# Performance work log

Hardware: AMD Instinct MI355X
Metric: run time of the kernel (lower is better)

The kernel has to match this reference:

```python
import jax, jax.numpy as jnp
import numpy as np

SCALE = 0.1
NUM_AA = 21  # num_aa + 1
NUM_RBF = 64
D_MIN, D_MAX = 0.0, 20.0
EPS = 1e-8


def _rbf(d):
    # d: [E] -> [E, NUM_RBF]
    mu = jnp.linspace(D_MIN, D_MAX, NUM_RBF, dtype=d.dtype)
    sigma = (D_MAX - D_MIN) / NUM_RBF
    return jnp.exp(-(((d[:, None] - mu) / sigma) ** 2))


def setup_inputs() -> dict:
    key = jax.random.key(0)
    k1, k2, k3, k4, k5 = jax.random.split(key, 5)
    N, E = 10000, 320000
    return {
        "decoded_atom14": jax.random.normal(k1, (N, 14, 3), dtype=jnp.float32),
        "rot": jax.random.normal(k2, (N, 3, 3), dtype=jnp.float32),
        "trans": jax.random.normal(k3, (N, 3), dtype=jnp.float32),
        "decoded_seq_logits": jax.random.normal(k4, (N, NUM_AA), dtype=jnp.float32),
        "edge_index": jax.random.randint(k5, (2, E), 0, N, dtype=jnp.int64)
        if jax.config.jax_enable_x64 else jax.random.randint(k5, (2, E), 0, N, dtype=jnp.int32),
    }


def reference(decoded_atom14, rot, trans, decoded_seq_logits, edge_index):
    E = edge_index.shape[1]
    dst = edge_index[0]
    src = edge_index[1]

    atom14 = decoded_atom14 * SCALE          # [N,14,3]
    t = trans * SCALE                        # [N,3] (scale_translation)

    seq = jnp.argmax(decoded_seq_logits, axis=-1)          # [N]
    src_seq = jax.nn.one_hot(seq[src], NUM_AA, dtype=jnp.float32)  # [E,21]
    dst_seq = jax.nn.one_hot(seq[dst], NUM_AA, dtype=jnp.float32)  # [E,21]

    X_ca = atom14[:, 1, :]                                  # [N,3]
    edge_dists = jnp.linalg.norm(X_ca[dst] - X_ca[src], axis=-1)   # [E]
    edge_rbf = _rbf(edge_dists)                             # [E,64]

    # invert_apply: R^T (x - t), per node, broadcast over 14 atoms
    local = jnp.einsum("nji,naj->nai", rot, atom14 - t[:, None, :])  # [N,14,3]
    src_atom14_local = local[src]                           # [E,14,3]
    dst_atom14_in_src_local = jnp.einsum(
        "eji,eaj->eai", rot[src], atom14[dst] - t[src][:, None, :]
    )                                                       # [E,14,3]

    # 14x14 pairwise distances (eps added to diff coords, as in original)
    diff = src_atom14_local[:, :, None, :] - dst_atom14_in_src_local[:, None, :, :] + EPS
    pair_dist = jnp.linalg.norm(diff, axis=-1)              # [E,14,14]

    return jnp.concatenate(
        [
            jnp.ones((E, 1), dtype=jnp.float32),
            src_seq,
            dst_seq,
            edge_rbf,
            src_atom14_local.reshape(E, -1),
            dst_atom14_in_src_local.reshape(E, -1),
            pair_dist.reshape(E, -1),
        ],
        axis=-1,
    ).astype(jnp.float32)
```

## Files before the change

### kernel.cpp

```cpp
#include <hip/hip_runtime.h>
#include <math.h>

#define NUM_AA   21
#define OUT_DIM  387
#define SCALE    0.1f
#define EPS_C    1e-8f
#define EPB      32
#define TPB      1024

typedef float v4f __attribute__((ext_vector_type(4)));

__global__ __launch_bounds__(256) void node_pre_kernel(
    const float* __restrict__ A, const float* __restrict__ R,
    const float* __restrict__ T, const float* __restrict__ LG,
    float* __restrict__ WS, int N)
{
    const int n = blockIdx.x * 256 + threadIdx.x;
    if (n >= N) return;

    float a14[42];
    #pragma unroll
    for (int k = 0; k < 42; ++k) a14[k] = A[(size_t)n * 42 + k] * SCALE;
    float rot[9];
    #pragma unroll
    for (int k = 0; k < 9; ++k) rot[k] = R[(size_t)n * 9 + k];
    const float t0 = T[(size_t)n * 3 + 0] * SCALE;
    const float t1 = T[(size_t)n * 3 + 1] * SCALE;
    const float t2 = T[(size_t)n * 3 + 2] * SCALE;

    const float* lg = LG + (size_t)n * NUM_AA;
    float best = lg[0]; int bi = 0;
    #pragma unroll
    for (int j = 1; j < NUM_AA; ++j) {
        float v = lg[j];
        if (v > best) { best = v; bi = j; }
    }

    float* S = WS + (size_t)n * 64;
    float* D = WS + (size_t)N * 64 + (size_t)n * 48;

    #pragma unroll
    for (int a = 0; a < 14; ++a) {
        const float x0 = a14[a * 3 + 0] - t0;
        const float x1 = a14[a * 3 + 1] - t1;
        const float x2 = a14[a * 3 + 2] - t2;
        #pragma unroll
        for (int i = 0; i < 3; ++i)
            S[a * 3 + i] = rot[i] * x0 + rot[3 + i] * x1 + rot[6 + i] * x2;
    }
    #pragma unroll
    for (int k = 0; k < 9; ++k) S[42 + k] = rot[k];
    S[51] = t0; S[52] = t1; S[53] = t2;
    S[54] = a14[3]; S[55] = a14[4]; S[56] = a14[5];
    S[57] = (float)bi;
    #pragma unroll
    for (int k = 58; k < 64; ++k) S[k] = 0.f;

    #pragma unroll
    for (int k = 0; k < 42; ++k) D[k] = a14[k];
    D[42] = a14[3]; D[43] = a14[4]; D[44] = a14[5];
    D[45] = (float)bi;
    D[46] = 0.f; D[47] = 0.f;
}

__device__ __forceinline__ void edge_phase1(const float* __restrict__ gs,
                                            float* __restrict__ row, int lane)
{
    {
        const float dx = gs[106] - gs[54];
        const float dy = gs[107] - gs[55];
        const float dz = gs[108] - gs[56];
        const float dca = __builtin_amdgcn_sqrtf(dx * dx + dy * dy + dz * dz);
        const float mu  = (float)lane * (20.0f / 63.0f);
        const float z   = (dca - mu) * 3.2f;
        row[43 + lane] = __expf(-z * z);
    }
    const int seqS = (int)gs[57];
    const int seqD = (int)gs[109];
    if (lane == 21) row[0] = 1.0f;
    if (lane < 21) {
        row[1  + lane] = (lane == seqS) ? 1.0f : 0.0f;
        row[22 + lane] = (lane == seqD) ? 1.0f : 0.0f;
    }
    if (lane < 42) {
        const int a = lane / 3;
        const int i = lane - a * 3;
        const float r0 = gs[42 + i], r1 = gs[45 + i], r2 = gs[48 + i];
        const float locD = r0 * (gs[64 + a * 3 + 0] - gs[51])
                         + r1 * (gs[64 + a * 3 + 1] - gs[52])
                         + r2 * (gs[64 + a * 3 + 2] - gs[53]);
        row[107 + lane] = gs[lane];
        row[149 + lane] = locD;
    }
}

__device__ __forceinline__ void edge_phase2(float* __restrict__ row, int lane)
{
    #pragma unroll
    for (int k = 0; k < 4; ++k) {
        const int p = lane + k * 64;
        if (p < 196) {
            const unsigned a = (unsigned)p / 14u;
            const unsigned b = (unsigned)p - a * 14u;
            const float ddx = row[107 + a * 3 + 0] - row[149 + b * 3 + 0] + EPS_C;
            const float ddy = row[107 + a * 3 + 1] - row[149 + b * 3 + 1] + EPS_C;
            const float ddz = row[107 + a * 3 + 2] - row[149 + b * 3 + 2] + EPS_C;
            row[191 + p] = __builtin_amdgcn_sqrtf(ddx * ddx + ddy * ddy + ddz * ddz);
        }
    }
}

__global__ __launch_bounds__(1024, 2) void edge_feat_kernel(
    const int*   __restrict__ EI,
    const float* __restrict__ WS,
    float* __restrict__ out,
    int E, int N)
{
    __shared__ __align__(16) float rowsh[EPB * OUT_DIM];
    __shared__ __align__(16) float gsh[16][224];

    const int wv   = threadIdx.x >> 6;
    const int lane = threadIdx.x & 63;
    const int eb   = blockIdx.x * EPB + wv * 2;

    int dst0, src0, dst1, src1;
    if (eb + 1 < E) {
        const int2 d = *reinterpret_cast<const int2*>(EI + eb);
        const int2 s = *reinterpret_cast<const int2*>(EI + E + eb);
        dst0 = d.x; dst1 = d.y; src0 = s.x; src1 = s.y;
    } else {
        const int e0c = (eb < E) ? eb : E - 1;
        dst0 = EI[e0c]; src0 = EI[E + e0c];
        dst1 = dst0; src1 = src0;
    }

    float* row0 = rowsh + (size_t)(wv * 2) * OUT_DIM;
    float* row1 = row0 + OUT_DIM;
    float* gs   = gsh[wv];

    {
        const int k   = (lane >= 28) ? 1 : 0;
        const int lr  = lane - k * 28;
        const bool isD = lr >= 16;
        const int sub = isD ? lr - 16 : lr;
        const int node = isD ? (k ? dst1 : dst0) : (k ? src1 : src0);
        const float* p = isD
            ? WS + (size_t)N * 64 + (size_t)node * 48 + sub * 4
            : WS + (size_t)node * 64 + sub * 4;
        if (lane < 56) {
            const v4f v = *reinterpret_cast<const v4f*>(p);
            *reinterpret_cast<v4f*>(&gs[k * 112 + (isD ? 64 : 0) + sub * 4]) = v;
        }
    }
    asm volatile("s_waitcnt lgkmcnt(0)" ::: "memory");
    __builtin_amdgcn_sched_barrier(0);

    edge_phase1(gs,       row0, lane);
    edge_phase1(gs + 112, row1, lane);
    asm volatile("s_waitcnt lgkmcnt(0)" ::: "memory");
    __builtin_amdgcn_sched_barrier(0);

    edge_phase2(row0, lane);
    edge_phase2(row1, lane);

    asm volatile("s_waitcnt lgkmcnt(0)" ::: "memory");
    __builtin_amdgcn_s_barrier();
    __builtin_amdgcn_sched_barrier(0);

    const long long base = (long long)blockIdx.x * (EPB * OUT_DIM);
    float* ob = out + base;
    const long long remain = (long long)E * OUT_DIM - base;

    if (remain >= (long long)(EPB * OUT_DIM)) {
        const v4f* s4 = reinterpret_cast<const v4f*>(rowsh);
        v4f* o4 = reinterpret_cast<v4f*>(ob);
        #pragma unroll
        for (int r = 0; r < 4; ++r) {
            const int q = threadIdx.x + r * TPB;
            if (q < (EPB * OUT_DIM) / 4)
                o4[q] = s4[q];
        }
    } else if (remain > 0) {
        for (int q = threadIdx.x; q < (int)remain; q += TPB)
            ob[q] = rowsh[q];
    }
}

extern "C" void kernel_launch(void* const* d_in, const int* in_sizes, int n_in,
                              void* d_out, int out_size, void* d_ws, size_t ws_size,
                              hipStream_t stream) {
    const float* A  = (const float*)d_in[0];
    const float* R  = (const float*)d_in[1];
    const float* T  = (const float*)d_in[2];
    const float* LG = (const float*)d_in[3];
    const int*   EI = (const int*)d_in[4];
    float* out = (float*)d_out;
    float* WS  = (float*)d_ws;

    const int N = in_sizes[0] / 42;
    const int E = in_sizes[4] / 2;

    node_pre_kernel<<<(N + 255) / 256, 256, 0, stream>>>(A, R, T, LG, WS, N);

    const int blocks = (E + EPB - 1) / EPB;
    edge_feat_kernel<<<blocks, TPB, 0, stream>>>(EI, WS, out, E, N);
}
```

Measured before the change: 129.0 us.

## Use per-wave output stores with small blocks, drop block barrier, nontemporal writes

Shrinks blocks from 1024 to 256 threads (8 edges each). Each wave now writes its own two edge rows directly to global memory, so the block-wide barrier is no longer needed. The stores become float2 nontemporal writes instead of block-cooperative float4 copies. This removes the cross-wave synchronisation and allows more resident blocks, at the cost of narrower vector stores and more blocks to schedule.

```diff
diff --git a/kernel.cpp b/kernel.cpp
--- a/kernel.cpp
+++ b/kernel.cpp
@@ -5,10 +5,11 @@
 #define OUT_DIM  387
 #define SCALE    0.1f
 #define EPS_C    1e-8f
-#define EPB      32
-#define TPB      1024
+#define EPB      8
+#define TPB      256
 
 typedef float v4f __attribute__((ext_vector_type(4)));
+typedef float v2f __attribute__((ext_vector_type(2)));
 
 __global__ __launch_bounds__(256) void node_pre_kernel(
     const float* __restrict__ A, const float* __restrict__ R,
@@ -110,18 +111,19 @@
     }
 }
 
-__global__ __launch_bounds__(1024, 2) void edge_feat_kernel(
+__global__ __launch_bounds__(256, 8) void edge_feat_kernel(
     const int*   __restrict__ EI,
     const float* __restrict__ WS,
     float* __restrict__ out,
     int E, int N)
 {
     __shared__ __align__(16) float rowsh[EPB * OUT_DIM];
-    __shared__ __align__(16) float gsh[16][224];
+    __shared__ __align__(16) float gsh[4][224];
 
     const int wv   = threadIdx.x >> 6;
     const int lane = threadIdx.x & 63;
     const int eb   = blockIdx.x * EPB + wv * 2;
+    if (eb >= E) return;
 
     int dst0, src0, dst1, src1;
     if (eb + 1 < E) {
@@ -129,8 +131,7 @@
         const int2 s = *reinterpret_cast<const int2*>(EI + E + eb);
         dst0 = d.x; dst1 = d.y; src0 = s.x; src1 = s.y;
     } else {
-        const int e0c = (eb < E) ? eb : E - 1;
-        dst0 = EI[e0c]; src0 = EI[E + e0c];
+        dst0 = EI[eb]; src0 = EI[E + eb];
         dst1 = dst0; src1 = src0;
     }
 
@@ -162,27 +163,25 @@
 
     edge_phase2(row0, lane);
     edge_phase2(row1, lane);
-
     asm volatile("s_waitcnt lgkmcnt(0)" ::: "memory");
-    __builtin_amdgcn_s_barrier();
     __builtin_amdgcn_sched_barrier(0);
 
-    const long long base = (long long)blockIdx.x * (EPB * OUT_DIM);
-    float* ob = out + base;
-    const long long remain = (long long)E * OUT_DIM - base;
-
-    if (remain >= (long long)(EPB * OUT_DIM)) {
-        const v4f* s4 = reinterpret_cast<const v4f*>(rowsh);
-        v4f* o4 = reinterpret_cast<v4f*>(ob);
+    const long long fbase = (long long)eb * OUT_DIM;
+    const long long remF  = (long long)E * OUT_DIM - fbase;
+    float* ob = out + fbase;
+
+    if (remF >= 2LL * OUT_DIM) {
+        const v2f* s2 = reinterpret_cast<const v2f*>(row0);
+        v2f* o2 = reinterpret_cast<v2f*>(ob);
         #pragma unroll
-        for (int r = 0; r < 4; ++r) {
-            const int q = threadIdx.x + r * TPB;
-            if (q < (EPB * OUT_DIM) / 4)
-                o4[q] = s4[q];
+        for (int k = 0; k < 7; ++k) {
+            const int q = lane + k * 64;
+            if (q < OUT_DIM)
+                __builtin_nontemporal_store(s2[q], o2 + q);
         }
-    } else if (remain > 0) {
-        for (int q = threadIdx.x; q < (int)remain; q += TPB)
-            ob[q] = rowsh[q];
+    } else {
+        for (int q = lane; q < (int)remF; q += 64)
+            __builtin_nontemporal_store(row0[q], ob + q);
     }
 }
 
```

After: 123.9 us. 4.0% less time.
